# Optimization experiments

Hardware: AMD Instinct MI355X
Metric: run time of the kernel (lower is better)

The kernel has to match this reference:

```python
import jax, jax.numpy as jnp
import numpy as np

N, E = 20000, 320000
H1, C1 = 8, 128   # gat1 heads/out
H2, C2 = 1, 128   # gat2 heads/out
D_IN = 768
NEG_SLOPE = 0.2
BN_EPS = 1e-5


def setup_inputs() -> dict:
    key = jax.random.key(0)
    ks = jax.random.split(key, 16)
    def rn(k, shape, fan):
        return jax.random.normal(k, shape, dtype=jnp.float32) / np.sqrt(fan)
    x = jax.random.normal(ks[0], (N, D_IN), dtype=jnp.float32)
    edge_index = jax.random.randint(ks[1], (2, E), 0, N, dtype=jnp.int64)
    return {
        "x": x,
        "edge_index": edge_index,
        "W1": rn(ks[2], (D_IN, H1 * C1), D_IN),
        "att_src1": rn(ks[3], (H1, C1), C1),
        "att_dst1": rn(ks[4], (H1, C1), C1),
        "b1": jnp.zeros((H1 * C1,), jnp.float32),
        "W2": rn(ks[5], (H1 * C1, H2 * C2), H1 * C1),
        "att_src2": rn(ks[6], (H2, C2), C2),
        "att_dst2": rn(ks[7], (H2, C2), C2),
        "b2": jnp.zeros((C2,), jnp.float32),
        "g1": jnp.ones((H1 * C1,), jnp.float32),
        "be1": jnp.zeros((H1 * C1,), jnp.float32),
        "g2": jnp.ones((C2,), jnp.float32),
        "be2": jnp.zeros((C2,), jnp.float32),
        "Wc1": rn(ks[8], (C2, 64), C2),
        "bc1": jnp.zeros((64,), jnp.float32),
        "Wc2": rn(ks[9], (64, 2), 64),
        "bc2": jnp.zeros((2,), jnp.float32),
    }


def gat_conv(x, src, dst, W, att_src, att_dst, bias, heads, ch, concat):
    n = x.shape[0]
    h = (x @ W).reshape(n, heads, ch)                      # [N,H,C]
    a_s = jnp.sum(h * att_src[None], axis=-1)              # [N,H]
    a_d = jnp.sum(h * att_dst[None], axis=-1)
    e = a_s[src] + a_d[dst]                                # [Et,H]
    e = jax.nn.leaky_relu(e, NEG_SLOPE)
    # segment softmax over incoming edges of each dst node
    m = jax.ops.segment_max(e, dst, num_segments=n)
    ex = jnp.exp(e - m[dst])
    z = jax.ops.segment_sum(ex, dst, num_segments=n)
    alpha = ex / z[dst]                                    # [Et,H]
    msg = alpha[:, :, None] * h[src]                       # [Et,H,C]
    out = jax.ops.segment_sum(msg, dst, num_segments=n)    # [N,H,C]
    if concat:
        out = out.reshape(n, heads * ch)
    else:
        out = out.mean(axis=1)
    return out + bias


def batch_norm(x, gamma, beta):
    mu = x.mean(axis=0)
    var = x.var(axis=0)
    return (x - mu) * jax.lax.rsqrt(var + BN_EPS) * gamma + beta


def reference(x, edge_index, W1, att_src1, att_dst1, b1, W2, att_src2, att_dst2, b2,
              g1, be1, g2, be2, Wc1, bc1, Wc2, bc2):
    n = x.shape[0]
    loop = jnp.arange(n, dtype=edge_index.dtype)
    src = jnp.concatenate([edge_index[0], loop])  # PyG add_self_loops default
    dst = jnp.concatenate([edge_index[1], loop])
    h = gat_conv(x, src, dst, W1, att_src1, att_dst1, b1, H1, C1, True)
    h = jax.nn.elu(batch_norm(h, g1, be1))
    h = gat_conv(h, src, dst, W2, att_src2, att_dst2, b2, H2, C2, False)
    h = jax.nn.elu(batch_norm(h, g2, be2))
    h = jax.nn.relu(h @ Wc1 + bc1)
    return h @ Wc2 + bc2
```

## Files before the change

### kernel.cpp

```cpp
#include <hip/hip_runtime.h>
#include <hip/hip_bf16.h>
#include <math.h>

#define N_NODES 20000
#define N_EDGES 320000
#define DIN 768
#define F1 1024
#define H1 8
#define C1 128
#define F2 128
#define NEG_SLOPE 0.2f
#define BN_EPS 1e-5f

typedef __attribute__((ext_vector_type(8))) __bf16 bf16x8;
typedef __attribute__((ext_vector_type(4))) float f32x4;

__device__ __forceinline__ float leaky(float x) { return x > 0.f ? x : NEG_SLOPE * x; }

__device__ __forceinline__ unsigned short f2bu(float x) {
  __hip_bfloat16 b = __float2bfloat16(x);
  return *(unsigned short*)&b;
}
__device__ __forceinline__ float b2f(unsigned short u) {
  return __uint_as_float(((unsigned)u) << 16);
}

__device__ __forceinline__ void async_copy16(void* lds, const void* g) {
  __builtin_amdgcn_global_load_lds(
      (const __attribute__((address_space(1))) unsigned int*)g,
      (__attribute__((address_space(3))) unsigned int*)lds, 16, 0, 0);
}

__global__ void repack_kernel(const int* raw, int* ei32) {
  int is64 = (raw[1] == 0 && raw[3] == 0 && raw[5] == 0 && raw[7] == 0) ? 1 : 0;
  int e = blockIdx.x * blockDim.x + threadIdx.x;
  if (e < 2 * N_EDGES) {
    ei32[e] = is64 ? raw[2 * e] : raw[e];
  }
}

__global__ void hist_kernel(const int* ei, int* deg) {
  int e = blockIdx.x * blockDim.x + threadIdx.x;
  if (e < N_EDGES) atomicAdd(&deg[ei[N_EDGES + e]], 1);
}

__global__ void scan_kernel(const int* deg, int* off, int* cursor) {
  __shared__ int tmp[1024];
  __shared__ int carry;
  if (threadIdx.x == 0) carry = 0;
  __syncthreads();
  for (int base = 0; base < N_NODES; base += 1024) {
    int i = base + threadIdx.x;
    int v = (i < N_NODES) ? deg[i] : 0;
    tmp[threadIdx.x] = v;
    __syncthreads();
    for (int s = 1; s < 1024; s <<= 1) {
      int t = (threadIdx.x >= s) ? tmp[threadIdx.x - s] : 0;
      __syncthreads();
      tmp[threadIdx.x] += t;
      __syncthreads();
    }
    int excl = tmp[threadIdx.x] - v;
    if (i < N_NODES) { int o = carry + excl; off[i] = o; cursor[i] = o; }
    __syncthreads();
    if (threadIdx.x == 1023) carry += tmp[1023];
    __syncthreads();
  }
  if (threadIdx.x == 0) off[N_NODES] = carry;
}

__global__ void scatter_kernel(const int* ei, int* cursor, int* elist) {
  int e = blockIdx.x * blockDim.x + threadIdx.x;
  if (e < N_EDGES) {
    int dst = ei[N_EDGES + e];
    int p = atomicAdd(&cursor[dst], 1);
    elist[p] = ei[e];
  }
}

__global__ void f2b_kernel(const float* __restrict__ in, unsigned short* __restrict__ out,
                           size_t n4) {
  size_t i = (size_t)blockIdx.x * blockDim.x + threadIdx.x;
  size_t stride = (size_t)gridDim.x * blockDim.x;
  for (; i < n4; i += stride) {
    float4 v = ((const float4*)in)[i];
    ushort4 u;
    u.x = f2bu(v.x); u.y = f2bu(v.y); u.z = f2bu(v.z); u.w = f2bu(v.w);
    ((ushort4*)out)[i] = u;
  }
}

__global__ void transpose_b_kernel(const float* __restrict__ W, unsigned short* __restrict__ WT,
                                   int K, int N) {
  __shared__ float t[32][33];
  int k0 = blockIdx.y * 32, n0 = blockIdx.x * 32;
  int tx = threadIdx.x & 31, ty = threadIdx.x >> 5;
  for (int i = 0; i < 32; i += 8)
    t[ty + i][tx] = W[(size_t)(k0 + ty + i) * N + n0 + tx];
  __syncthreads();
  for (int i = 0; i < 32; i += 8)
    WT[(size_t)(n0 + ty + i) * K + k0 + tx] = f2bu(t[tx][ty + i]);
}

#define GBM 128
#define GBN 128
#define GBK 64
template <int H>
__global__ __launch_bounds__(256) void mfma_gemm_att_kernel(
    const unsigned short* __restrict__ A,
    const unsigned short* __restrict__ BT,
    unsigned short* __restrict__ C,
    const float* __restrict__ att_src,
    const float* __restrict__ att_dst,
    float* __restrict__ as_out,
    float* __restrict__ ad_out,
    int M, int N, int K) {
  __shared__ __hip_bfloat16 As[GBM][GBK];
  __shared__ __hip_bfloat16 Bs[GBN][GBK];
  __shared__ float sred[128][2];
  __shared__ float dred[128][2];
  int tid = threadIdx.x;
  int lane = tid & 63, wid = tid >> 6;
  int wr = wid >> 1, wc = wid & 1;
  int row0 = blockIdx.y * GBM, col0 = blockIdx.x * GBN;
  int head = blockIdx.x;
  int l16 = lane & 15, l4 = lane >> 4;
  f32x4 acc[4][4] = {};
  for (int k0 = 0; k0 < K; k0 += GBK) {
#pragma unroll
    for (int j = 0; j < 4; ++j) {
      int c = j * 256 + tid;
      int r = c >> 3, kk = (c & 7) << 3;
      int ga = row0 + r; if (ga >= M) ga = M - 1;
      async_copy16(&As[r][kk], A + (size_t)ga * K + k0 + kk);
      async_copy16(&Bs[r][kk], BT + (size_t)(col0 + r) * K + k0 + kk);
    }
    __syncthreads();
#pragma unroll
    for (int ks = 0; ks < 2; ++ks) {
      bf16x8 af[4], bfr[4];
#pragma unroll
      for (int i = 0; i < 4; ++i)
        af[i] = *(const bf16x8*)&As[wr * 64 + i * 16 + l16][ks * 32 + l4 * 8];
#pragma unroll
      for (int j = 0; j < 4; ++j)
        bfr[j] = *(const bf16x8*)&Bs[wc * 64 + j * 16 + l16][ks * 32 + l4 * 8];
#pragma unroll
      for (int i = 0; i < 4; ++i)
#pragma unroll
        for (int j = 0; j < 4; ++j)
          acc[i][j] = __builtin_amdgcn_mfma_f32_16x16x32_bf16(af[i], bfr[j], acc[i][j], 0, 0, 0);
    }
    __syncthreads();
  }
#pragma unroll
  for (int i = 0; i < 4; ++i) {
#pragma unroll
    for (int j = 0; j < 4; ++j) {
#pragma unroll
      for (int r = 0; r < 4; ++r) {
        int row = row0 + wr * 64 + i * 16 + l4 * 4 + r;
        int col = col0 + wc * 64 + j * 16 + l16;
        if (row < M) C[(size_t)row * N + col] = f2bu(acc[i][j][r]);
      }
    }
  }
  float avs[4], avd[4];
#pragma unroll
  for (int j = 0; j < 4; ++j) {
    int col = col0 + wc * 64 + j * 16 + l16;
    avs[j] = att_src[col];
    avd[j] = att_dst[col];
  }
#pragma unroll
  for (int i = 0; i < 4; ++i) {
#pragma unroll
    for (int r = 0; r < 4; ++r) {
      float ps = 0.f, pd = 0.f;
#pragma unroll
      for (int j = 0; j < 4; ++j) { ps += acc[i][j][r] * avs[j]; pd += acc[i][j][r] * avd[j]; }
#pragma unroll
      for (int mk = 1; mk < 16; mk <<= 1) {
        ps += __shfl_xor(ps, mk, 64);
        pd += __shfl_xor(pd, mk, 64);
      }
      if (l16 == 0) {
        int lr = wr * 64 + i * 16 + l4 * 4 + r;
        sred[lr][wc] = ps;
        dred[lr][wc] = pd;
      }
    }
  }
  __syncthreads();
  if (tid < 128) {
    int row = row0 + tid;
    if (row < M) {
      as_out[(size_t)row * H + head] = sred[tid][0] + sred[tid][1];
      ad_out[(size_t)row * H + head] = dred[tid][0] + dred[tid][1];
    }
  }
}

__global__ __launch_bounds__(256) void gather1_kernel(const unsigned short* __restrict__ h1,
                                                      const float* __restrict__ as1,
                                                      const float* __restrict__ ad1,
                                                      const int* __restrict__ off,
                                                      const int* __restrict__ elist,
                                                      const float* __restrict__ b1,
                                                      unsigned short* __restrict__ out1) {
  int node = blockIdx.x;
  int tid = threadIdx.x;
  int head = tid >> 5;
  float ad = ad1[node * H1 + head];
  float as_self = as1[node * H1 + head];
  int s = off[node], e = off[node + 1];
  float m = leaky(as_self + ad);
  for (int i = s; i < e; ++i) {
    int src = elist[i];
    m = fmaxf(m, leaky(as1[src * H1 + head] + ad));
  }
  float a0 = 0.f, a1 = 0.f, a2 = 0.f, a3 = 0.f, z = 0.f;
  {
    float w = __expf(leaky(as_self + ad) - m);
    z += w;
    ushort4 hv = *(const ushort4*)(h1 + (size_t)node * F1 + tid * 4);
    a0 += w * b2f(hv.x); a1 += w * b2f(hv.y); a2 += w * b2f(hv.z); a3 += w * b2f(hv.w);
  }
  for (int i = s; i < e; ++i) {
    int src = elist[i];
    float w = __expf(leaky(as1[src * H1 + head] + ad) - m);
    z += w;
    ushort4 hv = *(const ushort4*)(h1 + (size_t)src * F1 + tid * 4);
    a0 += w * b2f(hv.x); a1 += w * b2f(hv.y); a2 += w * b2f(hv.z); a3 += w * b2f(hv.w);
  }
  float inv = 1.f / z;
  ushort4 o;
  o.x = f2bu(a0 * inv + b1[tid * 4 + 0]);
  o.y = f2bu(a1 * inv + b1[tid * 4 + 1]);
  o.z = f2bu(a2 * inv + b1[tid * 4 + 2]);
  o.w = f2bu(a3 * inv + b1[tid * 4 + 3]);
  *(ushort4*)(out1 + (size_t)node * F1 + tid * 4) = o;
}

__global__ void bnstats_bf16_kernel(const unsigned short* __restrict__ x,
                                    float* __restrict__ sums,
                                    int nrows, int F, int rowsPerBlock) {
  int tid = threadIdx.x;
  int c = tid * 4;
  int r0 = blockIdx.x * rowsPerBlock;
  int rend = min(r0 + rowsPerBlock, nrows);
  float s0 = 0.f, s1 = 0.f, s2 = 0.f, s3 = 0.f;
  float q0 = 0.f, q1 = 0.f, q2 = 0.f, q3 = 0.f;
  for (int r = r0; r < rend; ++r) {
    ushort4 u = *(const ushort4*)(x + (size_t)r * F + c);
    float v0 = b2f(u.x), v1 = b2f(u.y), v2 = b2f(u.z), v3 = b2f(u.w);
    s0 += v0; s1 += v1; s2 += v2; s3 += v3;
    q0 += v0 * v0; q1 += v1 * v1; q2 += v2 * v2; q3 += v3 * v3;
  }
  atomicAdd(&sums[c + 0], s0); atomicAdd(&sums[c + 1], s1);
  atomicAdd(&sums[c + 2], s2); atomicAdd(&sums[c + 3], s3);
  atomicAdd(&sums[F + c + 0], q0); atomicAdd(&sums[F + c + 1], q1);
  atomicAdd(&sums[F + c + 2], q2); atomicAdd(&sums[F + c + 3], q3);
}

template <int CPT>
__global__ void bnstats_kernel(const float* __restrict__ x, float* __restrict__ sums,
                               int nrows, int F, int rowsPerBlock) {
  int tid = threadIdx.x;
  int r0 = blockIdx.x * rowsPerBlock;
  int rend = min(r0 + rowsPerBlock, nrows);
  float s[CPT], q[CPT];
#pragma unroll
  for (int k = 0; k < CPT; ++k) { s[k] = 0.f; q[k] = 0.f; }
  for (int r = r0; r < rend; ++r) {
    const float* row = x + (size_t)r * F;
#pragma unroll
    for (int k = 0; k < CPT; ++k) {
      float v = row[tid + k * blockDim.x];
      s[k] += v; q[k] += v * v;
    }
  }
#pragma unroll
  for (int k = 0; k < CPT; ++k) {
    atomicAdd(&sums[tid + k * blockDim.x], s[k]);
    atomicAdd(&sums[F + tid + k * blockDim.x], q[k]);
  }
}

__global__ void bnfinal_kernel(const float* __restrict__ sums, const float* __restrict__ g,
                               const float* __restrict__ be, float* __restrict__ ss, int F) {
  int c = blockIdx.x * blockDim.x + threadIdx.x;
  if (c < F) {
    float mu = sums[c] * (1.f / N_NODES);
    float var = sums[F + c] * (1.f / N_NODES) - mu * mu;
    float sc = g[c] * rsqrtf(var + BN_EPS);
    ss[c] = sc;
    ss[F + c] = be[c] - mu * sc;
  }
}

__global__ void bnapply_bf16_kernel(unsigned short* __restrict__ x, const float* __restrict__ ss,
                                    int F, size_t total4) {
  size_t i = (size_t)blockIdx.x * blockDim.x + threadIdx.x;
  size_t stride = (size_t)gridDim.x * blockDim.x;
  for (; i < total4; i += stride) {
    int c = (int)((i * 4) & (size_t)(F - 1));
    ushort4 u = ((ushort4*)x)[i];
    float v0 = b2f(u.x) * ss[c + 0] + ss[F + c + 0];
    float v1 = b2f(u.y) * ss[c + 1] + ss[F + c + 1];
    float v2 = b2f(u.z) * ss[c + 2] + ss[F + c + 2];
    float v3 = b2f(u.w) * ss[c + 3] + ss[F + c + 3];
    v0 = v0 > 0.f ? v0 : expm1f(v0);
    v1 = v1 > 0.f ? v1 : expm1f(v1);
    v2 = v2 > 0.f ? v2 : expm1f(v2);
    v3 = v3 > 0.f ? v3 : expm1f(v3);
    u.x = f2bu(v0); u.y = f2bu(v1); u.z = f2bu(v2); u.w = f2bu(v3);
    ((ushort4*)x)[i] = u;
  }
}

__global__ void bnapply_kernel(float* __restrict__ x, const float* __restrict__ ss,
                               int F, size_t total4) {
  size_t i = (size_t)blockIdx.x * blockDim.x + threadIdx.x;
  size_t stride = (size_t)gridDim.x * blockDim.x;
  for (; i < total4; i += stride) {
    int c = (int)((i * 4) & (size_t)(F - 1));
    float4 v = ((float4*)x)[i];
    v.x = v.x * ss[c + 0] + ss[F + c + 0];
    v.y = v.y * ss[c + 1] + ss[F + c + 1];
    v.z = v.z * ss[c + 2] + ss[F + c + 2];
    v.w = v.w * ss[c + 3] + ss[F + c + 3];
    v.x = v.x > 0.f ? v.x : expm1f(v.x);
    v.y = v.y > 0.f ? v.y : expm1f(v.y);
    v.z = v.z > 0.f ? v.z : expm1f(v.z);
    v.w = v.w > 0.f ? v.w : expm1f(v.w);
    ((float4*)x)[i] = v;
  }
}

__global__ __launch_bounds__(64) void gather2_kernel(const unsigned short* __restrict__ h2,
                                                     const float* __restrict__ as2,
                                                     const float* __restrict__ ad2,
                                                     const int* __restrict__ off,
                                                     const int* __restrict__ elist,
                                                     const float* __restrict__ b2,
                                                     float* __restrict__ out2) {
  int node = blockIdx.x;
  int tid = threadIdx.x;
  float ad = ad2[node];
  float as_self = as2[node];
  int s = off[node], e = off[node + 1];
  float m = leaky(as_self + ad);
  for (int i = s; i < e; ++i) m = fmaxf(m, leaky(as2[elist[i]] + ad));
  float a0 = 0.f, a1 = 0.f, z = 0.f;
  {
    float w = __expf(leaky(as_self + ad) - m);
    z += w;
    ushort2 hv = *(const ushort2*)(h2 + (size_t)node * F2 + tid * 2);
    a0 += w * b2f(hv.x); a1 += w * b2f(hv.y);
  }
  for (int i = s; i < e; ++i) {
    int src = elist[i];
    float w = __expf(leaky(as2[src] + ad) - m);
    z += w;
    ushort2 hv = *(const ushort2*)(h2 + (size_t)src * F2 + tid * 2);
    a0 += w * b2f(hv.x); a1 += w * b2f(hv.y);
  }
  float inv = 1.f / z;
  float2 o = make_float2(a0 * inv + b2[tid * 2 + 0], a1 * inv + b2[tid * 2 + 1]);
  *(float2*)(out2 + (size_t)node * F2 + tid * 2) = o;
}

__global__ __launch_bounds__(64) void cls_kernel(const float* __restrict__ h,
                                                 const float* __restrict__ Wc1,
                                                 const float* __restrict__ bc1,
                                                 const float* __restrict__ Wc2,
                                                 const float* __restrict__ bc2,
                                                 float* __restrict__ out) {
  __shared__ float hl[128];
  int node = blockIdx.x;
  int tid = threadIdx.x;
  hl[tid] = h[(size_t)node * F2 + tid];
  hl[tid + 64] = h[(size_t)node * F2 + 64 + tid];
  __syncthreads();
  float acc = bc1[tid];
#pragma unroll
  for (int k = 0; k < 128; ++k) acc += hl[k] * Wc1[k * 64 + tid];
  acc = fmaxf(acc, 0.f);
  float2 w = *(const float2*)(Wc2 + tid * 2);
  float o0 = acc * w.x, o1 = acc * w.y;
  for (int sh = 32; sh >= 1; sh >>= 1) {
    o0 += __shfl_down(o0, sh, 64);
    o1 += __shfl_down(o1, sh, 64);
  }
  if (tid == 0) {
    out[node * 2 + 0] = o0 + bc2[0];
    out[node * 2 + 1] = o1 + bc2[1];
  }
}

extern "C" void kernel_launch(void* const* d_in, const int* in_sizes, int n_in,
                              void* d_out, int out_size, void* d_ws, size_t ws_size,
                              hipStream_t stream) {
  const float* x        = (const float*)d_in[0];
  const int*   ei_raw   = (const int*)d_in[1];
  const float* W1       = (const float*)d_in[2];
  const float* att_src1 = (const float*)d_in[3];
  const float* att_dst1 = (const float*)d_in[4];
  const float* b1       = (const float*)d_in[5];
  const float* W2       = (const float*)d_in[6];
  const float* att_src2 = (const float*)d_in[7];
  const float* att_dst2 = (const float*)d_in[8];
  const float* b2       = (const float*)d_in[9];
  const float* g1       = (const float*)d_in[10];
  const float* be1      = (const float*)d_in[11];
  const float* g2       = (const float*)d_in[12];
  const float* be2      = (const float*)d_in[13];
  const float* Wc1      = (const float*)d_in[14];
  const float* bc1      = (const float*)d_in[15];
  const float* Wc2      = (const float*)d_in[16];
  const float* bc2      = (const float*)d_in[17];
  float* out = (float*)d_out;

  char* ws = (char*)d_ws;
  size_t o = 0;
  unsigned short* h1b   = (unsigned short*)(ws + o); o += (size_t)N_NODES * F1 * 2;
  unsigned short* out1b = (unsigned short*)(ws + o); o += (size_t)N_NODES * F1 * 2;
  unsigned short* xb    = (unsigned short*)(ws + o); o += (size_t)N_NODES * DIN * 2;
  unsigned short* h2b   = (unsigned short*)(ws + o); o += (size_t)N_NODES * F2 * 2;
  float* out2  = (float*)(ws + o); o += (size_t)N_NODES * F2 * 4;
  float* as1   = (float*)(ws + o); o += (size_t)N_NODES * H1 * 4;
  float* ad1   = (float*)(ws + o); o += (size_t)N_NODES * H1 * 4;
  float* as2   = (float*)(ws + o); o += (size_t)N_NODES * 4;
  float* ad2   = (float*)(ws + o); o += (size_t)N_NODES * 4;
  char*  zbase = ws + o;
  float* bnsum1 = (float*)(ws + o); o += F1 * 2 * 4;
  float* bnsum2 = (float*)(ws + o); o += F2 * 2 * 4;
  int*   deg    = (int*)(ws + o); o += (size_t)N_NODES * 4;
  size_t zbytes = (size_t)((ws + o) - zbase);
  int*   offv   = (int*)(ws + o); o += (size_t)(N_NODES + 4) * 4;
  int*   cursor = (int*)(ws + o); o += (size_t)N_NODES * 4;
  int*   elist  = (int*)(ws + o); o += (size_t)N_EDGES * 4;
  float* ss1    = (float*)(ws + o); o += F1 * 2 * 4;
  float* ss2    = (float*)(ws + o); o += F2 * 2 * 4;
  int*   ei32   = (int*)(ws + o); o += (size_t)2 * N_EDGES * 4;
  unsigned short* W1T = (unsigned short*)(ws + o); o += (size_t)F1 * DIN * 2;
  unsigned short* W2T = (unsigned short*)(ws + o); o += (size_t)F2 * F1 * 2;
  (void)ws_size; (void)in_sizes; (void)n_in; (void)out_size;

  hipMemsetAsync((void*)zbase, 0, zbytes, stream);

  f2b_kernel<<<2048, 256, 0, stream>>>(x, xb, (size_t)N_NODES * DIN / 4);
  {
    dim3 g1d(F1 / 32, DIN / 32);
    transpose_b_kernel<<<g1d, 256, 0, stream>>>(W1, W1T, DIN, F1);
    dim3 g2d(F2 / 32, F1 / 32);
    transpose_b_kernel<<<g2d, 256, 0, stream>>>(W2, W2T, F1, F2);
  }

  repack_kernel<<<(2 * N_EDGES + 255) / 256, 256, 0, stream>>>(ei_raw, ei32);
  hist_kernel<<<(N_EDGES + 255) / 256, 256, 0, stream>>>(ei32, deg);
  scan_kernel<<<1, 1024, 0, stream>>>(deg, offv, cursor);
  scatter_kernel<<<(N_EDGES + 255) / 256, 256, 0, stream>>>(ei32, cursor, elist);

  {
    dim3 grid(F1 / GBN, (N_NODES + GBM - 1) / GBM);
    mfma_gemm_att_kernel<H1><<<grid, 256, 0, stream>>>(
        xb, W1T, h1b, att_src1, att_dst1, as1, ad1, N_NODES, F1, DIN);
  }
  gather1_kernel<<<N_NODES, 256, 0, stream>>>(h1b, as1, ad1, offv, elist, b1, out1b);
  {
    int rows = 79;
    int grid = (N_NODES + rows - 1) / rows;
    bnstats_bf16_kernel<<<grid, 256, 0, stream>>>(out1b, bnsum1, N_NODES, F1, rows);
  }
  bnfinal_kernel<<<(F1 + 255) / 256, 256, 0, stream>>>(bnsum1, g1, be1, ss1, F1);
  bnapply_bf16_kernel<<<2048, 256, 0, stream>>>(out1b, ss1, F1, (size_t)N_NODES * F1 / 4);

  {
    dim3 grid(F2 / GBN, (N_NODES + GBM - 1) / GBM);
    mfma_gemm_att_kernel<1><<<grid, 256, 0, stream>>>(
        out1b, W2T, h2b, att_src2, att_dst2, as2, ad2, N_NODES, F2, F1);
  }
  gather2_kernel<<<N_NODES, 64, 0, stream>>>(h2b, as2, ad2, offv, elist, b2, out2);
  {
    int rows = 79;
    int grid = (N_NODES + rows - 1) / rows;
    bnstats_kernel<1><<<grid, 128, 0, stream>>>(out2, bnsum2, N_NODES, F2, rows);
  }
  bnfinal_kernel<<<1, F2, 0, stream>>>(bnsum2, g2, be2, ss2, F2);
  bnapply_kernel<<<1024, 256, 0, stream>>>(out2, ss2, F2, (size_t)N_NODES * F2 / 4);

  cls_kernel<<<N_NODES, 64, 0, stream>>>(out2, Wc1, bc1, Wc2, bc2, out);
}
```

Measured before the change: 495.7 us.

## Use single-pass online softmax in GAT gathers, widen loads, rewrite scan

The two GAT gather kernels now compute the segment softmax in a single pass with an online max and lazy rescaling (only when a new logit exceeds the running max by a threshold). This removes the separate max pass over neighbour logits. Gather1 now uses 128 threads, each loading 8 bf16 values with 16-byte loads, and the next edge's index and logit are prefetched. The single-block scan is replaced by a per-thread serial scan followed by wavefront shuffle scans, which cuts barrier count. The thresholded rescale lets weights grow up to e^8 before correction, a small numerical tradeoff.

```diff
diff --git a/kernel.cpp b/kernel.cpp
--- a/kernel.cpp
+++ b/kernel.cpp
@@ -11,6 +11,7 @@
 #define F2 128
 #define NEG_SLOPE 0.2f
 #define BN_EPS 1e-5f
+#define RESCALE_THR 8.0f
 
 typedef __attribute__((ext_vector_type(8))) __bf16 bf16x8;
 typedef __attribute__((ext_vector_type(4))) float f32x4;
@@ -23,6 +24,9 @@
 }
 __device__ __forceinline__ float b2f(unsigned short u) {
   return __uint_as_float(((unsigned)u) << 16);
+}
+__device__ __forceinline__ unsigned pack2(float lo, float hi) {
+  return (unsigned)f2bu(lo) | ((unsigned)f2bu(hi) << 16);
 }
 
 __device__ __forceinline__ void async_copy16(void* lds, const void* g) {
@@ -44,29 +48,51 @@
   if (e < N_EDGES) atomicAdd(&deg[ei[N_EDGES + e]], 1);
 }
 
-__global__ void scan_kernel(const int* deg, int* off, int* cursor) {
-  __shared__ int tmp[1024];
-  __shared__ int carry;
-  if (threadIdx.x == 0) carry = 0;
+#define NPT 20
+__global__ __launch_bounds__(1024) void scan_kernel(const int* __restrict__ deg,
+                                                    int* __restrict__ off,
+                                                    int* __restrict__ cursor) {
+  __shared__ int wsum[16];
+  int tid = threadIdx.x;
+  int lane = tid & 63, wv = tid >> 6;
+  int base = tid * NPT;
+  int loc[NPT];
+  int run = 0;
+#pragma unroll
+  for (int k = 0; k < NPT; ++k) {
+    int i = base + k;
+    int v = (i < N_NODES) ? deg[i] : 0;
+    loc[k] = run;
+    run += v;
+  }
+  int incl = run;
+  for (int sh = 1; sh < 64; sh <<= 1) {
+    int t = __shfl_up(incl, sh, 64);
+    if (lane >= sh) incl += t;
+  }
+  if (lane == 63) wsum[wv] = incl;
   __syncthreads();
-  for (int base = 0; base < N_NODES; base += 1024) {
-    int i = base + threadIdx.x;
-    int v = (i < N_NODES) ? deg[i] : 0;
-    tmp[threadIdx.x] = v;
-    __syncthreads();
-    for (int s = 1; s < 1024; s <<= 1) {
-      int t = (threadIdx.x >= s) ? tmp[threadIdx.x - s] : 0;
-      __syncthreads();
-      tmp[threadIdx.x] += t;
-      __syncthreads();
-    }
-    int excl = tmp[threadIdx.x] - v;
-    if (i < N_NODES) { int o = carry + excl; off[i] = o; cursor[i] = o; }
-    __syncthreads();
-    if (threadIdx.x == 1023) carry += tmp[1023];
-    __syncthreads();
-  }
-  if (threadIdx.x == 0) off[N_NODES] = carry;
+  if (wv == 0 && lane < 16) {
+    int v = wsum[lane];
+    for (int sh = 1; sh < 16; sh <<= 1) {
+      int t = __shfl_up(v, sh, 16);
+      if (lane >= sh) v += t;
+    }
+    wsum[lane] = v;
+  }
+  __syncthreads();
+  int wbase = (wv > 0) ? wsum[wv - 1] : 0;
+  int tbase = wbase + incl - run;
+#pragma unroll
+  for (int k = 0; k < NPT; ++k) {
+    int i = base + k;
+    if (i < N_NODES) {
+      int o = tbase + loc[k];
+      off[i] = o;
+      cursor[i] = o;
+    }
+  }
+  if (tid == 1023) off[N_NODES] = wbase + incl;
 }
 
 __global__ void scatter_kernel(const int* ei, int* cursor, int* elist) {
@@ -201,7 +227,7 @@
   }
 }
 
-__global__ __launch_bounds__(256) void gather1_kernel(const unsigned short* __restrict__ h1,
+__global__ __launch_bounds__(128) void gather1_kernel(const unsigned short* __restrict__ h1,
                                                       const float* __restrict__ as1,
                                                       const float* __restrict__ ad1,
                                                       const int* __restrict__ off,
@@ -210,36 +236,52 @@
                                                       unsigned short* __restrict__ out1) {
   int node = blockIdx.x;
   int tid = threadIdx.x;
-  int head = tid >> 5;
+  int head = tid >> 4;
   float ad = ad1[node * H1 + head];
-  float as_self = as1[node * H1 + head];
   int s = off[node], e = off[node + 1];
-  float m = leaky(as_self + ad);
+  float m = leaky(as1[node * H1 + head] + ad);
+  float z = 1.f;
+  float acc[8];
+  {
+    uint4 u = *(const uint4*)(h1 + (size_t)node * F1 + tid * 8);
+    acc[0] = __uint_as_float(u.x << 16); acc[1] = __uint_as_float(u.x & 0xffff0000u);
+    acc[2] = __uint_as_float(u.y << 16); acc[3] = __uint_as_float(u.y & 0xffff0000u);
+    acc[4] = __uint_as_float(u.z << 16); acc[5] = __uint_as_float(u.z & 0xffff0000u);
+    acc[6] = __uint_as_float(u.w << 16); acc[7] = __uint_as_float(u.w & 0xffff0000u);
+  }
+  int src_n = 0; float e_n = 0.f;
+  if (s < e) { src_n = elist[s]; e_n = leaky(as1[src_n * H1 + head] + ad); }
   for (int i = s; i < e; ++i) {
-    int src = elist[i];
-    m = fmaxf(m, leaky(as1[src * H1 + head] + ad));
-  }
-  float a0 = 0.f, a1 = 0.f, a2 = 0.f, a3 = 0.f, z = 0.f;
-  {
-    float w = __expf(leaky(as_self + ad) - m);
+    int src = src_n;
+    float el = e_n;
+    if (i + 1 < e) { src_n = elist[i + 1]; e_n = leaky(as1[src_n * H1 + head] + ad); }
+    float w;
+    if (el > m + RESCALE_THR) {
+      float r = __expf(m - el);
+      z *= r;
+#pragma unroll
+      for (int k = 0; k < 8; ++k) acc[k] *= r;
+      m = el;
+      w = 1.f;
+    } else {
+      w = __expf(el - m);
+    }
     z += w;
-    ushort4 hv = *(const ushort4*)(h1 + (size_t)node * F1 + tid * 4);
-    a0 += w * b2f(hv.x); a1 += w * b2f(hv.y); a2 += w * b2f(hv.z); a3 += w * b2f(hv.w);
-  }
-  for (int i = s; i < e; ++i) {
-    int src = elist[i];
-    float w = __expf(leaky(as1[src * H1 + head] + ad) - m);
-    z += w;
-    ushort4 hv = *(const ushort4*)(h1 + (size_t)src * F1 + tid * 4);
-    a0 += w * b2f(hv.x); a1 += w * b2f(hv.y); a2 += w * b2f(hv.z); a3 += w * b2f(hv.w);
+    uint4 u = *(const uint4*)(h1 + (size_t)src * F1 + tid * 8);
+    acc[0] += w * __uint_as_float(u.x << 16); acc[1] += w * __uint_as_float(u.x & 0xffff0000u);
+    acc[2] += w * __uint_as_float(u.y << 16); acc[3] += w * __uint_as_float(u.y & 0xffff0000u);
+    acc[4] += w * __uint_as_float(u.z << 16); acc[5] += w * __uint_as_float(u.z & 0xffff0000u);
+    acc[6] += w * __uint_as_float(u.w << 16); acc[7] += w * __uint_as_float(u.w & 0xffff0000u);
   }
   float inv = 1.f / z;
-  ushort4 o;
-  o.x = f2bu(a0 * inv + b1[tid * 4 + 0]);
-  o.y = f2bu(a1 * inv + b1[tid * 4 + 1]);
-  o.z = f2bu(a2 * inv + b1[tid * 4 + 2]);
-  o.w = f2bu(a3 * inv + b1[tid * 4 + 3]);
-  *(ushort4*)(out1 + (size_t)node * F1 + tid * 4) = o;
+  const float4 bv0 = *(const float4*)(b1 + tid * 8);
+  const float4 bv1 = *(const float4*)(b1 + tid * 8 + 4);
+  uint4 o;
+  o.x = pack2(acc[0] * inv + bv0.x, acc[1] * inv + bv0.y);
+  o.y = pack2(acc[2] * inv + bv0.z, acc[3] * inv + bv0.w);
+  o.z = pack2(acc[4] * inv + bv1.x, acc[5] * inv + bv1.y);
+  o.w = pack2(acc[6] * inv + bv1.z, acc[7] * inv + bv1.w);
+  *(uint4*)(out1 + (size_t)node * F1 + tid * 8) = o;
 }
 
 __global__ void bnstats_bf16_kernel(const unsigned short* __restrict__ x,
@@ -348,23 +390,32 @@
   int node = blockIdx.x;
   int tid = threadIdx.x;
   float ad = ad2[node];
-  float as_self = as2[node];
   int s = off[node], e = off[node + 1];
-  float m = leaky(as_self + ad);
-  for (int i = s; i < e; ++i) m = fmaxf(m, leaky(as2[elist[i]] + ad));
-  float a0 = 0.f, a1 = 0.f, z = 0.f;
-  {
-    float w = __expf(leaky(as_self + ad) - m);
+  float m = leaky(as2[node] + ad);
+  float z = 1.f;
+  float a0, a1;
+  {
+    unsigned u = *(const unsigned*)(h2 + (size_t)node * F2 + tid * 2);
+    a0 = __uint_as_float(u << 16); a1 = __uint_as_float(u & 0xffff0000u);
+  }
+  int src_n = 0; float e_n = 0.f;
+  if (s < e) { src_n = elist[s]; e_n = leaky(as2[src_n] + ad); }
+  for (int i = s; i < e; ++i) {
+    int src = src_n;
+    float el = e_n;
+    if (i + 1 < e) { src_n = elist[i + 1]; e_n = leaky(as2[src_n] + ad); }
+    float w;
+    if (el > m + RESCALE_THR) {
+      float r = __expf(m - el);
+      z *= r; a0 *= r; a1 *= r;
+      m = el; w = 1.f;
+    } else {
+      w = __expf(el - m);
+    }
     z += w;
-    ushort2 hv = *(const ushort2*)(h2 + (size_t)node * F2 + tid * 2);
-    a0 += w * b2f(hv.x); a1 += w * b2f(hv.y);
-  }
-  for (int i = s; i < e; ++i) {
-    int src = elist[i];
-    float w = __expf(leaky(as2[src] + ad) - m);
-    z += w;
-    ushort2 hv = *(const ushort2*)(h2 + (size_t)src * F2 + tid * 2);
-    a0 += w * b2f(hv.x); a1 += w * b2f(hv.y);
+    unsigned u = *(const unsigned*)(h2 + (size_t)src * F2 + tid * 2);
+    a0 += w * __uint_as_float(u << 16);
+    a1 += w * __uint_as_float(u & 0xffff0000u);
   }
   float inv = 1.f / z;
   float2 o = make_float2(a0 * inv + b2[tid * 2 + 0], a1 * inv + b2[tid * 2 + 1]);
@@ -468,7 +519,7 @@
     mfma_gemm_att_kernel<H1><<<grid, 256, 0, stream>>>(
         xb, W1T, h1b, att_src1, att_dst1, as1, ad1, N_NODES, F1, DIN);
   }
-  gather1_kernel<<<N_NODES, 256, 0, stream>>>(h1b, as1, ad1, offv, elist, b1, out1b);
+  gather1_kernel<<<N_NODES, 128, 0, stream>>>(h1b, as1, ad1, offv, elist, b1, out1b);
   {
     int rows = 79;
     int grid = (N_NODES + rows - 1) / rows;
```

Result: faster. 452.3 us (-8.7%).
